# Kernel tuning notes

Hardware: AMD Instinct MI355X
Metric: run time of the kernel (lower is better)

## Reference

```python
import jax, jax.numpy as jnp
import numpy as np

B, NPG = 32, 4096   # graphs, nodes per graph (equal-size ragged segments)
F_IN, C, K, J = 64, 128, 32, 40
N_LAYERS = 3
EPS = 1e-5


def _global_layer_norm(x):
    # F.layer_norm(x, x.shape): normalize over ALL elements, no affine
    m = jnp.mean(x)
    v = jnp.mean(jnp.square(x - m))
    return (x - m) * jax.lax.rsqrt(v + EPS)


def setup_inputs() -> dict:
    key = jax.random.key(0)
    ks = jax.random.split(key, 7)
    N = B * NPG
    return {
        "node_feats": jax.random.normal(ks[0], (N, F_IN), jnp.float32),
        "frag_emb": jax.random.normal(ks[1], (B, J, F_IN), jnp.float32),
        "W_in": jax.random.normal(ks[2], (C, F_IN), jnp.float32) / np.sqrt(F_IN),
        "b_in": jnp.zeros((C,), jnp.float32),
        "U": jax.random.uniform(ks[3], (C, K), jnp.float32),
        "V": jax.random.uniform(ks[4], (C, K), jnp.float32),
        "q": jax.random.uniform(ks[5], (K,), jnp.float32),
        "gate_W": jax.random.normal(ks[6], (1, 2 * C), jnp.float32) / np.sqrt(2 * C),
        "gate_b": jnp.zeros((1,), jnp.float32),
    }


def reference(node_feats, frag_emb, W_in, b_in, U, V, q, gate_W, gate_b):
    # dropout is identity in eval mode
    xs = _global_layer_norm(node_feats @ W_in.T + b_in)      # [N, C]
    ys = _global_layer_norm(frag_emb @ W_in.T + b_in)        # [B, J, C]

    x = xs.reshape(B, NPG, C)                                # ragged segments -> [B, n, C]
    y_p = jax.nn.relu(jnp.einsum('bjd,dk->bjk', ys, V))      # [B, J, K]
    y_p = jax.nn.relu(q * y_p)

    I = x_p = None
    for il in range(N_LAYERS):
        x_p = jax.nn.relu(jnp.einsum('bid,dk->bik', x, U))   # [B, n, K]
        I = jnp.einsum('bik,bjk->bij', x_p, y_p)             # [B, n, J]
        if il < N_LAYERS - 1:
            A = jax.nn.softmax(I, axis=1)                    # softmax over nodes i
            h = jax.nn.relu(jnp.einsum('bij,bjk->bik', A, y_p))
            h = jnp.einsum('bik,dk->bid', h, V)              # [B, n, C]
            z = jax.nn.sigmoid(jnp.concatenate([x, h], -1) @ gate_W.T + gate_b)[..., 0]
            x = (1.0 - z)[..., None] * x + z[..., None] * h

    p = jnp.einsum('bij,bjk->bik', I, y_p)                   # [B, n, K]
    return jax.nn.sigmoid(jnp.einsum('bik,bik->bi', x_p, p)) # [B, n]
```

## Files before the change

kernel.cpp:

```cpp
#include <hip/hip_runtime.h>
#include <math.h>

namespace {
constexpr int BB = 32, NPG = 4096, NTOT = BB*NPG, C = 128, FIN = 64, KK = 32, JJ = 40;
constexpr int YROWS = BB*JJ;
constexpr float EPS = 1e-5f;

constexpr int CW_WU  = 0;
constexpr int CW_WV  = 2048;
constexpr int CW_VU  = 4096;
constexpr int CW_WG  = 5120;
constexpr int CW_VGX = 5184;
constexpr int CW_VGH = 5216;
constexpr int CW_CBU = 5248;
constexpr int CW_CSU = 5280;
constexpr int CW_CBV = 5312;
constexpr int CW_CSV = 5344;
constexpr int CW_SC  = 5376;
constexpr int CW_G   = 5384;
constexpr int CW_WB  = 9480;
constexpr int CW_SW  = 9544;
constexpr int CW_SB  = 9608;
constexpr int CW_SIZE = 9610;

constexpr size_t XU_OFF  = 0;
constexpr size_t GX_OFF  = XU_OFF + (size_t)NTOT*KK;
constexpr size_t YP_OFF  = GX_OFF + (size_t)NTOT;
constexpr size_t PMA_OFF = YP_OFF + (size_t)YROWS*KK;
constexpr size_t PSA_OFF = PMA_OFF + 81920;
constexpr size_t PMB_OFF = PSA_OFF + 81920;
constexpr size_t PSB_OFF = PMB_OFF + 81920;
constexpr size_t CWS_OFF = PSB_OFF + 81920;
constexpr size_t PBN_OFF = CWS_OFF + 9612;
constexpr size_t PBF_OFF = PBN_OFF + 2048;
constexpr size_t MS_OFF  = PBF_OFF + 80;
constexpr size_t ST_OFF  = MS_OFF + 2560;
constexpr size_t IBF_OFF = ST_OFF + 8;
}

#define ACC8(A, wv, u0, u1) do { \
  A[0] += (wv)*(u0).x; A[1] += (wv)*(u0).y; A[2] += (wv)*(u0).z; A[3] += (wv)*(u0).w; \
  A[4] += (wv)*(u1).x; A[5] += (wv)*(u1).y; A[6] += (wv)*(u1).z; A[7] += (wv)*(u1).w; } while(0)

__device__ __forceinline__ float dot4(const float4 a, const float4 b) {
  return a.x*b.x + a.y*b.y + a.z*b.z + a.w*b.w;
}
__device__ __forceinline__ float dot8v(const float x[8], const float4 y0, const float4 y1) {
  return x[0]*y0.x + x[1]*y0.y + x[2]*y0.z + x[3]*y0.w
       + x[4]*y1.x + x[5]*y1.y + x[6]*y1.z + x[7]*y1.w;
}
__device__ __forceinline__ float sigm(const float x) { return 1.f/(1.f + __expf(-x)); }

__global__ __launch_bounds__(256)
void k_pre(const float* __restrict__ W, const float* __restrict__ b,
           const float* __restrict__ U, const float* __restrict__ V,
           const float* __restrict__ gw, float* __restrict__ CWo) {
  __shared__ float W_l[128*64];
  __shared__ float V_l[128*32];
  const int t = threadIdx.x;
  for (int f = t; f < 2048; f += 256) *(float4*)(W_l + 4*f) = *(const float4*)(W + 4*f);
  if (blockIdx.x == 0)
    for (int f = t; f < 1024; f += 256) *(float4*)(V_l + 4*f) = *(const float4*)(V + 4*f);
  __syncthreads();
  if (blockIdx.x == 1) {
    const int d = t >> 2, e0 = (t & 3) * 16;
    float g[16];
    #pragma unroll
    for (int i = 0; i < 16; ++i) g[i] = 0.f;
    for (int c = 0; c < 128; ++c) {
      const float wv = W_l[c*64 + d];
      #pragma unroll
      for (int u = 0; u < 4; ++u) {
        const float4 we = *(const float4*)(W_l + c*64 + e0 + 4*u);
        g[4*u+0] += wv*we.x; g[4*u+1] += wv*we.y;
        g[4*u+2] += wv*we.z; g[4*u+3] += wv*we.w;
      }
    }
    #pragma unroll
    for (int u = 0; u < 4; ++u)
      *(float4*)(CWo + CW_G + d*64 + e0 + 4*u) = make_float4(g[4*u],g[4*u+1],g[4*u+2],g[4*u+3]);
    if (t < 64) {
      float awb = 0.f, asw = 0.f;
      for (int c = 0; c < 128; ++c) {
        const float wv = W_l[c*64 + t];
        awb += wv * b[c]; asw += wv;
      }
      CWo[CW_WB + t] = awb; CWo[CW_SW + t] = asw;
    }
    if (t == 0) {
      float sb = 0.f, sb2 = 0.f;
      for (int c = 0; c < 128; ++c) { sb += b[c]; sb2 += b[c]*b[c]; }
      CWo[CW_SB+0] = sb; CWo[CW_SB+1] = sb2;
    }
    return;
  }
  {
    const int d = t >> 2, k0 = (t & 3) * 8;
    float au[8] = {0,0,0,0,0,0,0,0};
    float av[8] = {0,0,0,0,0,0,0,0};
    for (int c = 0; c < 128; ++c) {
      const float wv = W_l[c*64 + d];
      const float4 u0 = *(const float4*)(U + c*32 + k0);
      const float4 u1 = *(const float4*)(U + c*32 + k0 + 4);
      ACC8(au, wv, u0, u1);
      const float4 v0 = *(const float4*)(V_l + c*32 + k0);
      const float4 v1 = *(const float4*)(V_l + c*32 + k0 + 4);
      ACC8(av, wv, v0, v1);
    }
    *(float4*)(CWo + CW_WU + d*32 + k0)     = make_float4(au[0],au[1],au[2],au[3]);
    *(float4*)(CWo + CW_WU + d*32 + k0 + 4) = make_float4(au[4],au[5],au[6],au[7]);
    *(float4*)(CWo + CW_WV + d*32 + k0)     = make_float4(av[0],av[1],av[2],av[3]);
    *(float4*)(CWo + CW_WV + d*32 + k0 + 4) = make_float4(av[4],av[5],av[6],av[7]);
  }
  if (t < 128) {
    const int kp = t >> 2, k0 = (t & 3) * 8;
    float a[8] = {0,0,0,0,0,0,0,0};
    for (int c = 0; c < 128; ++c) {
      const float vv = V_l[c*32 + kp];
      const float4 u0 = *(const float4*)(U + c*32 + k0);
      const float4 u1 = *(const float4*)(U + c*32 + k0 + 4);
      ACC8(a, vv, u0, u1);
    }
    *(float4*)(CWo + CW_VU + kp*32 + k0)     = make_float4(a[0],a[1],a[2],a[3]);
    *(float4*)(CWo + CW_VU + kp*32 + k0 + 4) = make_float4(a[4],a[5],a[6],a[7]);
  }
  if (t < 64) {
    float a = 0.f;
    for (int c = 0; c < 128; ++c) a += W_l[c*64 + t] * gw[c];
    CWo[CW_WG + t] = a;
  }
  if (t < 32) {
    float a1=0,a2=0,a3=0,a4=0,a5=0,a6=0;
    for (int c = 0; c < 128; ++c) {
      const float uv = U[c*32 + t], vv = V_l[c*32 + t], bc = b[c];
      a1 += vv*gw[c]; a2 += vv*gw[128+c];
      a3 += bc*uv;    a4 += uv;
      a5 += bc*vv;    a6 += vv;
    }
    CWo[CW_VGX+t]=a1; CWo[CW_VGH+t]=a2; CWo[CW_CBU+t]=a3; CWo[CW_CSU+t]=a4;
    CWo[CW_CBV+t]=a5; CWo[CW_CSV+t]=a6;
  }
  if (t == 0) {
    float bg=0.f, sg=0.f;
    for (int c = 0; c < 128; ++c) { bg += b[c]*gw[c]; sg += gw[c]; }
    CWo[CW_SC+0]=bg; CWo[CW_SC+1]=sg;
  }
}

__global__ __launch_bounds__(256,6)
void k_cov(const float* __restrict__ inp, const float* __restrict__ CW,
           double* __restrict__ PB, const int ntiles) {
  __shared__ float a_l[64*64];
  __shared__ float red[12];
  const int t = threadIdx.x;
  const int dg = t >> 4, eg = t & 15;
  const int d0 = dg*4, e0 = eg*4;
  float av1 = 0.f, av2 = 0.f, avb = 0.f;
  int nt = 0;
  for (int tile = blockIdx.x; tile < ntiles; tile += gridDim.x) {
    __syncthreads();
    const size_t r0 = (size_t)tile * 64;
    #pragma unroll
    for (int s = 0; s < 4; ++s) {
      int f = (t + 256*s) * 4;
      *(float4*)(a_l + f) = *(const float4*)(inp + r0*FIN + f);
    }
    __syncthreads();
    float S[4][4];
    #pragma unroll
    for (int i=0;i<4;i++)
      #pragma unroll
      for (int j=0;j<4;j++) S[i][j] = 0.f;
    float4 cs = make_float4(0.f,0.f,0.f,0.f);
    #pragma unroll 4
    for (int r = 0; r < 64; ++r) {
      const float4 ad = *(const float4*)(a_l + r*64 + d0);
      const float4 ae = *(const float4*)(a_l + r*64 + e0);
      S[0][0]+=ad.x*ae.x; S[0][1]+=ad.x*ae.y; S[0][2]+=ad.x*ae.z; S[0][3]+=ad.x*ae.w;
      S[1][0]+=ad.y*ae.x; S[1][1]+=ad.y*ae.y; S[1][2]+=ad.y*ae.z; S[1][3]+=ad.y*ae.w;
      S[2][0]+=ad.z*ae.x; S[2][1]+=ad.z*ae.y; S[2][2]+=ad.z*ae.z; S[2][3]+=ad.z*ae.w;
      S[3][0]+=ad.w*ae.x; S[3][1]+=ad.w*ae.y; S[3][2]+=ad.w*ae.z; S[3][3]+=ad.w*ae.w;
      cs.x += ad.x; cs.y += ad.y; cs.z += ad.z; cs.w += ad.w;
    }
    #pragma unroll
    for (int i = 0; i < 4; ++i) {
      const float4 g4 = *(const float4*)(CW + CW_G + (d0+i)*64 + e0);
      av2 += S[i][0]*g4.x + S[i][1]*g4.y + S[i][2]*g4.z + S[i][3]*g4.w;
    }
    if (eg == 0) {
      const float4 sw4 = *(const float4*)(CW + CW_SW + d0);
      const float4 wb4 = *(const float4*)(CW + CW_WB + d0);
      av1 += cs.x*sw4.x + cs.y*sw4.y + cs.z*sw4.z + cs.w*sw4.w;
      avb += cs.x*wb4.x + cs.y*wb4.y + cs.z*wb4.z + cs.w*wb4.w;
    }
    ++nt;
  }
  #pragma unroll
  for (int off = 32; off > 0; off >>= 1) {
    av2 += __shfl_xor(av2, off);
    av1 += __shfl_xor(av1, off);
    avb += __shfl_xor(avb, off);
  }
  const int w = t >> 6;
  if ((t & 63) == 0) { red[w*3] = av1; red[w*3+1] = av2; red[w*3+2] = avb; }
  __syncthreads();
  if (t == 0) {
    const float sb = CW[CW_SB], sb2 = CW[CW_SB+1];
    const double rowsB = 64.0 * (double)nt;
    const double s1 = (double)(red[0]+red[3]+red[6]+red[9]);
    const double s2 = (double)(red[1]+red[4]+red[7]+red[10]);
    const double sB = (double)(red[2]+red[5]+red[8]+red[11]);
    PB[(size_t)blockIdx.x*2 + 0] = s1 + rowsB*(double)sb;
    PB[(size_t)blockIdx.x*2 + 1] = s2 + 2.0*sB + rowsB*(double)sb2;
  }
}

__global__ __launch_bounds__(256)
void k_comb(const double* __restrict__ PBn, const double* __restrict__ PBf,
            double* __restrict__ ST) {
  __shared__ double red[8];
  const int t = threadIdx.x;
  double a = PBn[2*t] + PBn[2*(t+256)];
  double b = PBn[2*t+1] + PBn[2*(t+256)+1];
  #pragma unroll
  for (int off = 32; off > 0; off >>= 1) {
    a += __shfl_down(a, off);
    b += __shfl_down(b, off);
  }
  if ((t & 63) == 0) { red[(t>>6)*2] = a; red[(t>>6)*2+1] = b; }
  __syncthreads();
  if (t == 0) {
    ST[0] = red[0]+red[2]+red[4]+red[6];
    ST[1] = red[1]+red[3]+red[5]+red[7];
  }
  if (t < 64) {
    double c = (t < 20) ? PBf[2*t]   : 0.0;
    double d = (t < 20) ? PBf[2*t+1] : 0.0;
    #pragma unroll
    for (int off = 32; off > 0; off >>= 1) {
      c += __shfl_down(c, off);
      d += __shfl_down(d, off);
    }
    if (t == 0) { ST[2] = c; ST[3] = d; }
  }
}

__global__ __launch_bounds__(256)
void k_comb2(const float* __restrict__ Pm, const float* __restrict__ Ps,
             float* __restrict__ MS) {
  __shared__ float Mq[160], Sq[160], Msh[40];
  const int t = threadIdx.x;
  const int b = blockIdx.x;
  const int j = t >> 2, q = t & 3;
  float pm[16];
  if (t < 160) {
    float m = 0.f;
    #pragma unroll
    for (int u = 0; u < 16; ++u) {
      pm[u] = Pm[(size_t)b*2560 + j*64 + q*16 + u];
      m = fmaxf(m, pm[u]);
    }
    Mq[t] = m;
  }
  __syncthreads();
  if (t < 40) Msh[t] = fmaxf(fmaxf(Mq[4*t], Mq[4*t+1]), fmaxf(Mq[4*t+2], Mq[4*t+3]));
  __syncthreads();
  if (t < 160) {
    const float M = Msh[j];
    float s = 0.f;
    #pragma unroll
    for (int u = 0; u < 16; ++u)
      s += Ps[(size_t)b*2560 + j*64 + q*16 + u] * __expf(pm[u] - M);
    Sq[t] = s;
  }
  __syncthreads();
  if (t < 40) {
    const float S = Sq[4*t] + Sq[4*t+1] + Sq[4*t+2] + Sq[4*t+3];
    MS[(size_t)b*80 + t] = Msh[t];
    MS[(size_t)b*80 + 40 + t] = 1.f/S;
  }
}

__device__ __forceinline__ void irow_compute(const float* ypj, const float xp[8],
                                             const int kq, float4 p[10]) {
  #pragma unroll
  for (int m = 0; m < 10; ++m) {
    float4 acc;
    #pragma unroll
    for (int jj = 0; jj < 4; ++jj) {
      const int j = 4*m + jj;
      const float4 y0 = *(const float4*)(ypj + j*32 + kq*8);
      const float4 y1 = *(const float4*)(ypj + j*32 + kq*8 + 4);
      const float s = xp[0]*y0.x + xp[1]*y0.y + xp[2]*y0.z + xp[3]*y0.w
                    + xp[4]*y1.x + xp[5]*y1.y + xp[6]*y1.z + xp[7]*y1.w;
      if (jj==0) acc.x = s; else if (jj==1) acc.y = s; else if (jj==2) acc.z = s; else acc.w = s;
    }
    acc.x += __shfl_xor(acc.x,1); acc.x += __shfl_xor(acc.x,2);
    acc.y += __shfl_xor(acc.y,1); acc.y += __shfl_xor(acc.y,2);
    acc.z += __shfl_xor(acc.z,1); acc.z += __shfl_xor(acc.z,2);
    acc.w += __shfl_xor(acc.w,1); acc.w += __shfl_xor(acc.w,2);
    p[m] = acc;
  }
}

__device__ __forceinline__ void partials_out(const float4 p[10], const int t, const int kq,
    float* sredm, float* sreds, float* redm,
    float* __restrict__ PmB, float* __restrict__ PsB) {
  float ev[10];
  #pragma unroll
  for (int m = 0; m < 10; ++m) {
    const float4 qv = p[m];
    ev[m] = (kq&1) ? ((kq&2)? qv.w : qv.y) : ((kq&2)? qv.z : qv.x);
  }
  const int w = t >> 6, tl = t & 63;
  float mv[10];
  #pragma unroll
  for (int m = 0; m < 10; ++m) {
    mv[m] = ev[m];
    mv[m] = fmaxf(mv[m], __shfl_xor(mv[m], 4));
    mv[m] = fmaxf(mv[m], __shfl_xor(mv[m], 8));
    mv[m] = fmaxf(mv[m], __shfl_xor(mv[m], 16));
    mv[m] = fmaxf(mv[m], __shfl_xor(mv[m], 32));
  }
  if (tl < 4) {
    #pragma unroll
    for (int m = 0; m < 10; ++m) sredm[w*40 + 4*m + kq] = mv[m];
  }
  __syncthreads();
  if (t < 40)
    redm[t] = fmaxf(fmaxf(sredm[t], sredm[40+t]), fmaxf(sredm[80+t], sredm[120+t]));
  __syncthreads();
  float es[10];
  #pragma unroll
  for (int m = 0; m < 10; ++m) {
    const float M = redm[4*m + kq];
    es[m] = __expf(ev[m]-M);
    es[m] += __shfl_xor(es[m], 4);
    es[m] += __shfl_xor(es[m], 8);
    es[m] += __shfl_xor(es[m], 16);
    es[m] += __shfl_xor(es[m], 32);
  }
  if (tl < 4) {
    #pragma unroll
    for (int m = 0; m < 10; ++m) sreds[w*40 + 4*m + kq] = es[m];
  }
  __syncthreads();
  if (t < 40) {
    PmB[(size_t)t*64] = redm[t];
    PsB[(size_t)t*64] = sreds[t]+sreds[40+t]+sreds[80+t]+sreds[120+t];
  }
}

__device__ __forceinline__ void partials_lds(const float* p_l, const int t,
    float* sredm, float* sreds, float* redm,
    float* __restrict__ PmB, float* __restrict__ PsB) {
  const int r2 = t >> 2, kq = t & 3;
  const int w = t >> 6, tl = t & 63;
  float ev[10];
  #pragma unroll
  for (int m = 0; m < 10; ++m) ev[m] = p_l[r2*44 + 4*m + kq];
  float mv[10];
  #pragma unroll
  for (int m = 0; m < 10; ++m) {
    mv[m] = ev[m];
    mv[m] = fmaxf(mv[m], __shfl_xor(mv[m], 4));
    mv[m] = fmaxf(mv[m], __shfl_xor(mv[m], 8));
    mv[m] = fmaxf(mv[m], __shfl_xor(mv[m], 16));
    mv[m] = fmaxf(mv[m], __shfl_xor(mv[m], 32));
  }
  if (tl < 4) {
    #pragma unroll
    for (int m = 0; m < 10; ++m) sredm[w*40 + 4*m + kq] = mv[m];
  }
  __syncthreads();
  if (t < 40)
    redm[t] = fmaxf(fmaxf(sredm[t], sredm[40+t]), fmaxf(sredm[80+t], sredm[120+t]));
  __syncthreads();
  float es[10];
  #pragma unroll
  for (int m = 0; m < 10; ++m) {
    const float M = redm[4*m + kq];
    es[m] = __expf(ev[m]-M);
    es[m] += __shfl_xor(es[m], 4);
    es[m] += __shfl_xor(es[m], 8);
    es[m] += __shfl_xor(es[m], 16);
    es[m] += __shfl_xor(es[m], 32);
  }
  if (tl < 4) {
    #pragma unroll
    for (int m = 0; m < 10; ++m) sreds[w*40 + 4*m + kq] = es[m];
  }
  __syncthreads();
  if (t < 40) {
    PmB[(size_t)t*64] = redm[t];
    PsB[(size_t)t*64] = sreds[t]+sreds[40+t]+sreds[80+t]+sreds[120+t];
  }
}

__global__ __launch_bounds__(256,4)
void k_yp2(const float* __restrict__ fe, const float* __restrict__ CW,
           const float* __restrict__ q, const double* __restrict__ ST,
           float* __restrict__ yp) {
  __shared__ float in_t[64*64];
  __shared__ float Wl[64*32];
  const int t = threadIdx.x;
  const int r0 = blockIdx.x * 64;
  #pragma unroll
  for (int s = 0; s < 4; ++s) {
    int f = (t + 256*s) * 4;
    int r = f >> 6, d = f & 63;
    float4 v = *(const float4*)(fe + (size_t)r0*FIN + f);
    *(float4*)(in_t + r*64 + (d ^ ((r & 7) * 8))) = v;
  }
  #pragma unroll
  for (int s = 0; s < 2; ++s) {
    int f = (t + 256*s) * 4;
    *(float4*)(Wl + f) = *(const float4*)(CW + CW_WV + f);
  }
  __syncthreads();
  const double cy = (double)YROWS * (double)C;
  const double myd = ST[2]/cy, vy = ST[3]/cy - myd*myd;
  const float ry = (float)(1.0/sqrt(vy + (double)EPS));
  const float mr = (float)myd * ry;
  const int r2 = t >> 2, kq = t & 3;
  const int swz = (r2 & 7) * 8;
  float acc[8] = {0,0,0,0,0,0,0,0};
  #pragma unroll
  for (int dc = 0; dc < 16; ++dc) {
    const int d = dc*4;
    const float4 a = *(const float4*)(in_t + r2*64 + (d ^ swz));
    { const float4 w0 = *(const float4*)(Wl + (d+0)*32 + kq*8);
      const float4 w1 = *(const float4*)(Wl + (d+0)*32 + kq*8 + 4); ACC8(acc, a.x, w0, w1); }
    { const float4 w0 = *(const float4*)(Wl + (d+1)*32 + kq*8);
      const float4 w1 = *(const float4*)(Wl + (d+1)*32 + kq*8 + 4); ACC8(acc, a.y, w0, w1); }
    { const float4 w0 = *(const float4*)(Wl + (d+2)*32 + kq*8);
      const float4 w1 = *(const float4*)(Wl + (d+2)*32 + kq*8 + 4); ACC8(acc, a.z, w0, w1); }
    { const float4 w0 = *(const float4*)(Wl + (d+3)*32 + kq*8);
      const float4 w1 = *(const float4*)(Wl + (d+3)*32 + kq*8 + 4); ACC8(acc, a.w, w0, w1); }
  }
  #pragma unroll
  for (int i = 0; i < 8; ++i) {
    const int k = kq*8 + i;
    const float typ = ry*(acc[i] + CW[CW_CBV+k]) - mr*CW[CW_CSV+k];
    float v = fmaxf(typ, 0.f);
    acc[i] = fmaxf(q[k]*v, 0.f);
  }
  *(float4*)(yp + (size_t)(r0+r2)*KK + kq*8)     = make_float4(acc[0],acc[1],acc[2],acc[3]);
  *(float4*)(yp + (size_t)(r0+r2)*KK + kq*8 + 4) = make_float4(acc[4],acc[5],acc[6],acc[7]);
}

__global__ __launch_bounds__(256,4)
void k_I0b(const float* __restrict__ nf, const float* __restrict__ CW,
           const double* __restrict__ ST, const float* __restrict__ yp,
           float* __restrict__ XU, float* __restrict__ GX,
           float* __restrict__ Pm, float* __restrict__ Ps,
           float* __restrict__ Ibf) {
  __shared__ __align__(16) float in_t[64*68];
  __shared__ __align__(16) float Wl[64*36];
  __shared__ __align__(16) float ypj[40*40];
  __shared__ __align__(16) float wgl[64];
  __shared__ float sredm[160], sreds[160], redm[40];
  float* p_l = in_t;
  const int t = threadIdx.x;
  const int bid = blockIdx.x;
  const int b = bid >> 6, blk = bid & 63;
  const size_t rowbase = (size_t)b*NPG + (size_t)blk*64;
  #pragma unroll
  for (int s = 0; s < 4; ++s) {
    int f = (t + 256*s) * 4;
    int r = f >> 6, d = f & 63;
    *(float4*)(in_t + r*68 + d) = *(const float4*)(nf + rowbase*FIN + f);
  }
  #pragma unroll
  for (int s = 0; s < 2; ++s) {
    int idx = t + 256*s;
    int d = idx >> 3, kc = idx & 7;
    *(float4*)(Wl + ((d&15)*4 + (d>>4))*36 + kc*4) = *(const float4*)(CW + CW_WU + idx*4);
  }
  for (int f4v = t; f4v < 320; f4v += 256) {
    int j = f4v >> 3, kc = f4v & 7;
    *(float4*)(ypj + j*40 + kc*4) = *(const float4*)(yp + (size_t)b*(JJ*KK) + f4v*4);
  }
  if (t < 64) wgl[t] = CW[CW_WG + t];
  __syncthreads();
  const double cx = (double)NTOT * (double)C;
  const double mx = ST[0]/cx, vx = ST[1]/cx - mx*mx;
  const float rx = (float)(1.0/sqrt(vx + (double)EPS));
  const float mr = (float)mx * rx;
  const int kq = t & 3, X = (t >> 2) & 3, rr = t >> 4;
  float acc[4][8];
  #pragma unroll
  for (int i=0;i<4;i++)
    #pragma unroll
    for (int u=0;u<8;u++) acc[i][u] = 0.f;
  #pragma unroll
  for (int dd = 0; dd < 4; ++dd) {
    float4 a4[4];
    #pragma unroll
    for (int i = 0; i < 4; ++i)
      a4[i] = *(const float4*)(in_t + (rr+16*i)*68 + X*16 + dd*4);
    #pragma unroll
    for (int qd = 0; qd < 4; ++qd) {
      const int lrow = (dd*4 + qd)*4 + X;
      const float4 w0 = *(const float4*)(Wl + lrow*36 + kq*8);
      const float4 w1 = *(const float4*)(Wl + lrow*36 + kq*8 + 4);
      #pragma unroll
      for (int i = 0; i < 4; ++i) {
        const float av = (qd==0)? a4[i].x : (qd==1)? a4[i].y : (qd==2)? a4[i].z : a4[i].w;
        ACC8(acc[i], av, w0, w1);
      }
    }
  }
  #pragma unroll
  for (int i = 0; i < 4; ++i)
    #pragma unroll
    for (int u = 0; u < 8; ++u) {
      acc[i][u] += __shfl_xor(acc[i][u], 4);
      acc[i][u] += __shfl_xor(acc[i][u], 8);
    }
  float gp[4];
  #pragma unroll
  for (int i = 0; i < 4; ++i) {
    const float4 a = *(const float4*)(in_t + (rr+16*i)*68 + X*16 + kq*4);
    const float4 w = *(const float4*)(wgl + X*16 + kq*4);
    gp[i] = dot4(a, w);
    gp[i] += __shfl_xor(gp[i], 1);
    gp[i] += __shfl_xor(gp[i], 2);
    gp[i] += __shfl_xor(gp[i], 4);
    gp[i] += __shfl_xor(gp[i], 8);
  }
  const float4 cb0 = *(const float4*)(CW + CW_CBU + kq*8);
  const float4 cb1 = *(const float4*)(CW + CW_CBU + kq*8 + 4);
  const float4 cu0 = *(const float4*)(CW + CW_CSU + kq*8);
  const float4 cu1 = *(const float4*)(CW + CW_CSU + kq*8 + 4);
  float xp[4][8];
  #pragma unroll
  for (int i = 0; i < 4; ++i) {
    acc[i][0] = rx*(acc[i][0] + cb0.x) - mr*cu0.x;
    acc[i][1] = rx*(acc[i][1] + cb0.y) - mr*cu0.y;
    acc[i][2] = rx*(acc[i][2] + cb0.z) - mr*cu0.z;
    acc[i][3] = rx*(acc[i][3] + cb0.w) - mr*cu0.w;
    acc[i][4] = rx*(acc[i][4] + cb1.x) - mr*cu1.x;
    acc[i][5] = rx*(acc[i][5] + cb1.y) - mr*cu1.y;
    acc[i][6] = rx*(acc[i][6] + cb1.z) - mr*cu1.z;
    acc[i][7] = rx*(acc[i][7] + cb1.w) - mr*cu1.w;
    #pragma unroll
    for (int u = 0; u < 8; ++u) xp[i][u] = fmaxf(acc[i][u], 0.f);
  }
  if (X == 0) {
    const float bG = CW[CW_SC], sG = CW[CW_SC+1];
    #pragma unroll
    for (int i = 0; i < 4; ++i) {
      const size_t row = rowbase + rr + 16*i;
      *(float4*)(XU + row*KK + kq*8)     = make_float4(acc[i][0],acc[i][1],acc[i][2],acc[i][3]);
      *(float4*)(XU + row*KK + kq*8 + 4) = make_float4(acc[i][4],acc[i][5],acc[i][6],acc[i][7]);
      if (kq == 0) GX[row] = rx*(gp[i] + bG) - mr*sG;
    }
  }
  __syncthreads();
  #pragma unroll 2
  for (int jj = 0; jj < 10; ++jj) {
    const int j = X*10 + jj;
    const float4 y0 = *(const float4*)(ypj + j*40 + kq*8);
    const float4 y1 = *(const float4*)(ypj + j*40 + kq*8 + 4);
    float p4[4];
    #pragma unroll
    for (int i = 0; i < 4; ++i) p4[i] = dot8v(xp[i], y0, y1);
    #pragma unroll
    for (int i = 0; i < 4; ++i) {
      p4[i] += __shfl_xor(p4[i], 1);
      p4[i] += __shfl_xor(p4[i], 2);
    }
    if (kq == 0) {
      #pragma unroll
      for (int i = 0; i < 4; ++i)
        p_l[(rr+16*i)*44 + j] = p4[i];
    }
  }
  __syncthreads();
  partials_lds(p_l, t, sredm, sreds, redm,
               Pm + (size_t)b*2560 + blk, Ps + (size_t)b*2560 + blk);
  for (int f4v = t; f4v < 640; f4v += 256) {
    const int row = f4v / 10, jq = f4v - row*10;
    *(float4*)(Ibf + (rowbase+row)*JJ + jq*4) = *(const float4*)(p_l + row*44 + jq*4);
  }
}

template<int FINAL>
__global__ __launch_bounds__(256,4)
void k_fused6(float* __restrict__ XU, float* __restrict__ GX,
              float* __restrict__ Ibf,
              const float* __restrict__ yp, const float* __restrict__ CW,
              const float* __restrict__ gb, const float* __restrict__ MS,
              float* __restrict__ PmOut, float* __restrict__ PsOut,
              float* __restrict__ outp) {
  __shared__ float ypj[40*32];
  __shared__ float e_l[64*44];
  __shared__ float h_l[64*40];
  __shared__ float VUl[32*32];
  __shared__ float M_l[40], Si_l[40];
  __shared__ float vgxl[32], vghl[32];
  float* sredm = e_l;
  float* sreds = e_l + 160;
  float* redm  = e_l + 320;
  const int t = threadIdx.x;
  const int bid = blockIdx.x;
  const int b = bid >> 6, blk = bid & 63;
  const size_t rowbase = (size_t)b*NPG + (size_t)blk*64;
  for (int f4v = t; f4v < 320; f4v += 256)
    *(float4*)(ypj + f4v*4) = *(const float4*)(yp + (size_t)b*(JJ*KK) + f4v*4);
  { const int f = t*4;
    *(float4*)(VUl + f) = *(const float4*)(CW + CW_VU + f); }
  if (t < 32) { vgxl[t] = CW[CW_VGX+t]; vghl[t] = CW[CW_VGH+t]; }
  if (t < 40) { M_l[t] = MS[(size_t)b*80 + t]; Si_l[t] = MS[(size_t)b*80 + 40 + t]; }
  __syncthreads();
  for (int f4v = t; f4v < 640; f4v += 256) {
    const int row = f4v / 10, jq = f4v - row*10;
    const float4 iv = *(const float4*)(Ibf + (rowbase+row)*JJ + jq*4);
    float4 e4;
    e4.x = __expf(iv.x - M_l[jq*4+0]) * Si_l[jq*4+0];
    e4.y = __expf(iv.y - M_l[jq*4+1]) * Si_l[jq*4+1];
    e4.z = __expf(iv.z - M_l[jq*4+2]) * Si_l[jq*4+2];
    e4.w = __expf(iv.w - M_l[jq*4+3]) * Si_l[jq*4+3];
    *(float4*)(e_l + row*44 + jq*4) = e4;
  }
  const int r2 = t >> 2, kq = t & 3;
  float xu[8];
  {
    const float4 x0 = *(const float4*)(XU + (rowbase+r2)*KK + kq*8);
    const float4 x1 = *(const float4*)(XU + (rowbase+r2)*KK + kq*8 + 4);
    xu[0]=x0.x; xu[1]=x0.y; xu[2]=x0.z; xu[3]=x0.w;
    xu[4]=x1.x; xu[5]=x1.y; xu[6]=x1.z; xu[7]=x1.w;
  }
  const float gx = GX[rowbase + r2];
  __syncthreads();
  {
    const int rq = t >> 3, kc = t & 7;
    float4 h0 = make_float4(0.f,0.f,0.f,0.f), h1 = make_float4(0.f,0.f,0.f,0.f);
    #pragma unroll 4
    for (int j = 0; j < JJ; ++j) {
      const float4 yv = *(const float4*)(ypj + j*32 + kc*4);
      const float e0 = e_l[rq*44 + j];
      const float e1 = e_l[(rq+32)*44 + j];
      h0.x += e0*yv.x; h0.y += e0*yv.y; h0.z += e0*yv.z; h0.w += e0*yv.w;
      h1.x += e1*yv.x; h1.y += e1*yv.y; h1.z += e1*yv.z; h1.w += e1*yv.w;
    }
    h0.x = fmaxf(h0.x,0.f); h0.y = fmaxf(h0.y,0.f); h0.z = fmaxf(h0.z,0.f); h0.w = fmaxf(h0.w,0.f);
    h1.x = fmaxf(h1.x,0.f); h1.y = fmaxf(h1.y,0.f); h1.z = fmaxf(h1.z,0.f); h1.w = fmaxf(h1.w,0.f);
    *(float4*)(h_l + rq*40 + kc*4) = h0;
    *(float4*)(h_l + (rq+32)*40 + kc*4) = h1;
  }
  __syncthreads();
  float hu[8] = {0,0,0,0,0,0,0,0};
  float gh2 = 0.f, ghx = 0.f;
  #pragma unroll 8
  for (int kp = 0; kp < KK; ++kp) {
    const float hv = h_l[r2*40 + kp];
    gh2 += hv * vghl[kp];
    ghx += hv * vgxl[kp];
    const float4 v0 = *(const float4*)(VUl + kp*32 + kq*8);
    const float4 v1 = *(const float4*)(VUl + kp*32 + kq*8 + 4);
    ACC8(hu, hv, v0, v1);
  }
  const float z = 1.f/(1.f + __expf(-(gx + gh2 + gb[0])));
  float xp[8];
  #pragma unroll
  for (int i = 0; i < 8; ++i) {
    xu[i] = (1.f - z)*xu[i] + z*hu[i];
    xp[i] = fmaxf(xu[i], 0.f);
  }
  if (!FINAL) {
    *(float4*)(XU + (rowbase+r2)*KK + kq*8)     = make_float4(xu[0],xu[1],xu[2],xu[3]);
    *(float4*)(XU + (rowbase+r2)*KK + kq*8 + 4) = make_float4(xu[4],xu[5],xu[6],xu[7]);
    if (kq == 0) GX[rowbase + r2] = (1.f - z)*gx + z*ghx;
  }
  float4 p[10];
  irow_compute(ypj, xp, kq, p);
  if (FINAL) {
    float s = 0.f;
    #pragma unroll
    for (int m = 0; m < 10; ++m)
      s += p[m].x*p[m].x + p[m].y*p[m].y + p[m].z*p[m].z + p[m].w*p[m].w;
    if (kq == 0) outp[rowbase + r2] = 1.f/(1.f + __expf(-s));
    return;
  }
  #pragma unroll
  for (int m = 0; m < 10; ++m)
    if ((m & 3) == kq)
      *(float4*)(Ibf + (rowbase+r2)*JJ + 4*m) = p[m];
  partials_out(p, t, kq, sredm, sreds, redm,
               PmOut + (size_t)b*2560 + blk, PsOut + (size_t)b*2560 + blk);
}

extern "C" void kernel_launch(void* const* d_in, const int* in_sizes, int n_in,
                              void* d_out, int out_size, void* d_ws, size_t ws_size,
                              hipStream_t stream) {
  const float* nf  = (const float*)d_in[0];
  const float* fe  = (const float*)d_in[1];
  const float* W   = (const float*)d_in[2];
  const float* bin = (const float*)d_in[3];
  const float* U   = (const float*)d_in[4];
  const float* V   = (const float*)d_in[5];
  const float* q   = (const float*)d_in[6];
  const float* gw  = (const float*)d_in[7];
  const float* gb  = (const float*)d_in[8];
  float* out = (float*)d_out;
  float* wf  = (float*)d_ws;

  float* XU  = wf + XU_OFF;
  float* GX  = wf + GX_OFF;
  float* YP  = wf + YP_OFF;
  float* PMa = wf + PMA_OFF;
  float* PSa = wf + PSA_OFF;
  float* PMb = wf + PMB_OFF;
  float* PSb = wf + PSB_OFF;
  float* CWp = wf + CWS_OFF;
  float* MSb = wf + MS_OFF;
  float* IBF = wf + IBF_OFF;
  double* PBn = (double*)(wf + PBN_OFF);
  double* PBf = (double*)(wf + PBF_OFF);
  double* ST  = (double*)(wf + ST_OFF);

  k_pre<<<2, 256, 0, stream>>>(W, bin, U, V, gw, CWp);
  k_cov<<<512, 256, 0, stream>>>(nf, CWp, PBn, NTOT/64);
  k_cov<<<20, 256, 0, stream>>>(fe, CWp, PBf, YROWS/64);
  k_comb<<<1, 256, 0, stream>>>(PBn, PBf, ST);
  k_yp2<<<YROWS/64, 256, 0, stream>>>(fe, CWp, q, ST, YP);
  k_I0b<<<NTOT/64, 256, 0, stream>>>(nf, CWp, ST, YP, XU, GX, PMa, PSa, IBF);
  k_comb2<<<32, 256, 0, stream>>>(PMa, PSa, MSb);
  k_fused6<0><<<NTOT/64, 256, 0, stream>>>(XU, GX, IBF, YP, CWp, gb, MSb, PMb, PSb, nullptr);
  k_comb2<<<32, 256, 0, stream>>>(PMb, PSb, MSb);
  k_fused6<1><<<NTOT/64, 256, 0, stream>>>(XU, GX, IBF, YP, CWp, gb, MSb, nullptr, nullptr, out);
}
```

Measured before the change: 254.7 us.

## Fuse small reduction kernels into consumers and merge covariance launches

Merges the two covariance-statistics launches into one grid and folds the global-stats combine kernel into the consumers (yp and I0), where each block redoes the small reduction itself. The per-graph softmax max/sum combine kernel is likewise removed: each fused block recomputes M and 1/S from the partials, which are now stored in a block-major layout. The e matrix in LDS is transposed with padding to avoid bank conflicts. This cuts four launches and their serialization gaps, at the cost of redundant small reductions in every block of the large kernels.

```diff
diff --git a/kernel.cpp b/kernel.cpp
--- a/kernel.cpp
+++ b/kernel.cpp
@@ -33,9 +33,7 @@
 constexpr size_t CWS_OFF = PSB_OFF + 81920;
 constexpr size_t PBN_OFF = CWS_OFF + 9612;
 constexpr size_t PBF_OFF = PBN_OFF + 2048;
-constexpr size_t MS_OFF  = PBF_OFF + 80;
-constexpr size_t ST_OFF  = MS_OFF + 2560;
-constexpr size_t IBF_OFF = ST_OFF + 8;
+constexpr size_t IBF_OFF = PBF_OFF + 80;
 }
 
 #define ACC8(A, wv, u0, u1) do { \
@@ -148,16 +146,23 @@
 }
 
 __global__ __launch_bounds__(256,6)
-void k_cov(const float* __restrict__ inp, const float* __restrict__ CW,
-           double* __restrict__ PB, const int ntiles) {
+void k_cov2(const float* __restrict__ nf, const float* __restrict__ fe,
+            const float* __restrict__ CW,
+            double* __restrict__ PBn, double* __restrict__ PBf) {
   __shared__ float a_l[64*64];
   __shared__ float red[12];
   const int t = threadIdx.x;
+  const bool isNf = (blockIdx.x < 512);
+  const float* inp = isNf ? nf : fe;
+  double* PB = isNf ? PBn : PBf;
+  const int bid = isNf ? blockIdx.x : (blockIdx.x - 512);
+  const int ntiles = isNf ? (NTOT/64) : (YROWS/64);
+  const int gstr = isNf ? 512 : 20;
   const int dg = t >> 4, eg = t & 15;
   const int d0 = dg*4, e0 = eg*4;
   float av1 = 0.f, av2 = 0.f, avb = 0.f;
   int nt = 0;
-  for (int tile = blockIdx.x; tile < ntiles; tile += gridDim.x) {
+  for (int tile = bid; tile < ntiles; tile += gstr) {
     __syncthreads();
     const size_t r0 = (size_t)tile * 64;
     #pragma unroll
@@ -210,74 +215,8 @@
     const double s1 = (double)(red[0]+red[3]+red[6]+red[9]);
     const double s2 = (double)(red[1]+red[4]+red[7]+red[10]);
     const double sB = (double)(red[2]+red[5]+red[8]+red[11]);
-    PB[(size_t)blockIdx.x*2 + 0] = s1 + rowsB*(double)sb;
-    PB[(size_t)blockIdx.x*2 + 1] = s2 + 2.0*sB + rowsB*(double)sb2;
-  }
-}
-
-__global__ __launch_bounds__(256)
-void k_comb(const double* __restrict__ PBn, const double* __restrict__ PBf,
-            double* __restrict__ ST) {
-  __shared__ double red[8];
-  const int t = threadIdx.x;
-  double a = PBn[2*t] + PBn[2*(t+256)];
-  double b = PBn[2*t+1] + PBn[2*(t+256)+1];
-  #pragma unroll
-  for (int off = 32; off > 0; off >>= 1) {
-    a += __shfl_down(a, off);
-    b += __shfl_down(b, off);
-  }
-  if ((t & 63) == 0) { red[(t>>6)*2] = a; red[(t>>6)*2+1] = b; }
-  __syncthreads();
-  if (t == 0) {
-    ST[0] = red[0]+red[2]+red[4]+red[6];
-    ST[1] = red[1]+red[3]+red[5]+red[7];
-  }
-  if (t < 64) {
-    double c = (t < 20) ? PBf[2*t]   : 0.0;
-    double d = (t < 20) ? PBf[2*t+1] : 0.0;
-    #pragma unroll
-    for (int off = 32; off > 0; off >>= 1) {
-      c += __shfl_down(c, off);
-      d += __shfl_down(d, off);
-    }
-    if (t == 0) { ST[2] = c; ST[3] = d; }
-  }
-}
-
-__global__ __launch_bounds__(256)
-void k_comb2(const float* __restrict__ Pm, const float* __restrict__ Ps,
-             float* __restrict__ MS) {
-  __shared__ float Mq[160], Sq[160], Msh[40];
-  const int t = threadIdx.x;
-  const int b = blockIdx.x;
-  const int j = t >> 2, q = t & 3;
-  float pm[16];
-  if (t < 160) {
-    float m = 0.f;
-    #pragma unroll
-    for (int u = 0; u < 16; ++u) {
-      pm[u] = Pm[(size_t)b*2560 + j*64 + q*16 + u];
-      m = fmaxf(m, pm[u]);
-    }
-    Mq[t] = m;
-  }
-  __syncthreads();
-  if (t < 40) Msh[t] = fmaxf(fmaxf(Mq[4*t], Mq[4*t+1]), fmaxf(Mq[4*t+2], Mq[4*t+3]));
-  __syncthreads();
-  if (t < 160) {
-    const float M = Msh[j];
-    float s = 0.f;
-    #pragma unroll
-    for (int u = 0; u < 16; ++u)
-      s += Ps[(size_t)b*2560 + j*64 + q*16 + u] * __expf(pm[u] - M);
-    Sq[t] = s;
-  }
-  __syncthreads();
-  if (t < 40) {
-    const float S = Sq[4*t] + Sq[4*t+1] + Sq[4*t+2] + Sq[4*t+3];
-    MS[(size_t)b*80 + t] = Msh[t];
-    MS[(size_t)b*80 + 40 + t] = 1.f/S;
+    PB[(size_t)bid*2 + 0] = s1 + rowsB*(double)sb;
+    PB[(size_t)bid*2 + 1] = s2 + 2.0*sB + rowsB*(double)sb2;
   }
 }
 
@@ -346,8 +285,8 @@
   }
   __syncthreads();
   if (t < 40) {
-    PmB[(size_t)t*64] = redm[t];
-    PsB[(size_t)t*64] = sreds[t]+sreds[40+t]+sreds[80+t]+sreds[120+t];
+    PmB[t] = redm[t];
+    PsB[t] = sreds[t]+sreds[40+t]+sreds[80+t]+sreds[120+t];
   }
 }
 
@@ -392,17 +331,18 @@
   }
   __syncthreads();
   if (t < 40) {
-    PmB[(size_t)t*64] = redm[t];
-    PsB[(size_t)t*64] = sreds[t]+sreds[40+t]+sreds[80+t]+sreds[120+t];
+    PmB[t] = redm[t];
+    PsB[t] = sreds[t]+sreds[40+t]+sreds[80+t]+sreds[120+t];
   }
 }
 
 __global__ __launch_bounds__(256,4)
-void k_yp2(const float* __restrict__ fe, const float* __restrict__ CW,
-           const float* __restrict__ q, const double* __restrict__ ST,
+void k_yp3(const float* __restrict__ fe, const float* __restrict__ CW,
+           const float* __restrict__ q, const double* __restrict__ PBf,
            float* __restrict__ yp) {
   __shared__ float in_t[64*64];
   __shared__ float Wl[64*32];
+  __shared__ double fred[2];
   const int t = threadIdx.x;
   const int r0 = blockIdx.x * 64;
   #pragma unroll
@@ -417,9 +357,19 @@
     int f = (t + 256*s) * 4;
     *(float4*)(Wl + f) = *(const float4*)(CW + CW_WV + f);
   }
+  if (t < 64) {
+    double c = (t < 20) ? PBf[2*t]   : 0.0;
+    double d = (t < 20) ? PBf[2*t+1] : 0.0;
+    #pragma unroll
+    for (int off = 32; off > 0; off >>= 1) {
+      c += __shfl_down(c, off);
+      d += __shfl_down(d, off);
+    }
+    if (t == 0) { fred[0] = c; fred[1] = d; }
+  }
   __syncthreads();
   const double cy = (double)YROWS * (double)C;
-  const double myd = ST[2]/cy, vy = ST[3]/cy - myd*myd;
+  const double myd = fred[0]/cy, vy = fred[1]/cy - myd*myd;
   const float ry = (float)(1.0/sqrt(vy + (double)EPS));
   const float mr = (float)myd * ry;
   const int r2 = t >> 2, kq = t & 3;
@@ -450,8 +400,8 @@
 }
 
 __global__ __launch_bounds__(256,4)
-void k_I0b(const float* __restrict__ nf, const float* __restrict__ CW,
-           const double* __restrict__ ST, const float* __restrict__ yp,
+void k_I0c(const float* __restrict__ nf, const float* __restrict__ CW,
+           const double* __restrict__ PBn, const float* __restrict__ yp,
            float* __restrict__ XU, float* __restrict__ GX,
            float* __restrict__ Pm, float* __restrict__ Ps,
            float* __restrict__ Ibf) {
@@ -460,6 +410,7 @@
   __shared__ __align__(16) float ypj[40*40];
   __shared__ __align__(16) float wgl[64];
   __shared__ float sredm[160], sreds[160], redm[40];
+  __shared__ double dred[8];
   float* p_l = in_t;
   const int t = threadIdx.x;
   const int bid = blockIdx.x;
@@ -482,9 +433,21 @@
     *(float4*)(ypj + j*40 + kc*4) = *(const float4*)(yp + (size_t)b*(JJ*KK) + f4v*4);
   }
   if (t < 64) wgl[t] = CW[CW_WG + t];
-  __syncthreads();
+  {
+    double a = PBn[2*t] + PBn[2*(t+256)];
+    double bb = PBn[2*t+1] + PBn[2*(t+256)+1];
+    #pragma unroll
+    for (int off = 32; off > 0; off >>= 1) {
+      a  += __shfl_down(a, off);
+      bb += __shfl_down(bb, off);
+    }
+    if ((t & 63) == 0) { dred[(t>>6)*2] = a; dred[(t>>6)*2+1] = bb; }
+  }
+  __syncthreads();
+  const double ST0 = dred[0]+dred[2]+dred[4]+dred[6];
+  const double ST1 = dred[1]+dred[3]+dred[5]+dred[7];
   const double cx = (double)NTOT * (double)C;
-  const double mx = ST[0]/cx, vx = ST[1]/cx - mx*mx;
+  const double mx = ST0/cx, vx = ST1/cx - mx*mx;
   const float rx = (float)(1.0/sqrt(vx + (double)EPS));
   const float mr = (float)mx * rx;
   const int kq = t & 3, X = (t >> 2) & 3, rr = t >> 4;
@@ -579,7 +542,7 @@
   }
   __syncthreads();
   partials_lds(p_l, t, sredm, sreds, redm,
-               Pm + (size_t)b*2560 + blk, Ps + (size_t)b*2560 + blk);
+               Pm + ((size_t)b*64 + blk)*40, Ps + ((size_t)b*64 + blk)*40);
   for (int f4v = t; f4v < 640; f4v += 256) {
     const int row = f4v / 10, jq = f4v - row*10;
     *(float4*)(Ibf + (rowbase+row)*JJ + jq*4) = *(const float4*)(p_l + row*44 + jq*4);
@@ -588,21 +551,23 @@
 
 template<int FINAL>
 __global__ __launch_bounds__(256,4)
-void k_fused6(float* __restrict__ XU, float* __restrict__ GX,
+void k_fused7(float* __restrict__ XU, float* __restrict__ GX,
               float* __restrict__ Ibf,
               const float* __restrict__ yp, const float* __restrict__ CW,
-              const float* __restrict__ gb, const float* __restrict__ MS,
+              const float* __restrict__ gb,
+              const float* __restrict__ PmIn, const float* __restrict__ PsIn,
               float* __restrict__ PmOut, float* __restrict__ PsOut,
               float* __restrict__ outp) {
   __shared__ float ypj[40*32];
-  __shared__ float e_l[64*44];
+  __shared__ float eT[40*65];
   __shared__ float h_l[64*40];
   __shared__ float VUl[32*32];
   __shared__ float M_l[40], Si_l[40];
   __shared__ float vgxl[32], vghl[32];
-  float* sredm = e_l;
-  float* sreds = e_l + 160;
-  float* redm  = e_l + 320;
+  __shared__ float Mq[160], Sq[160];
+  float* sredm = eT;
+  float* sreds = eT + 160;
+  float* redm  = eT + 320;
   const int t = threadIdx.x;
   const int bid = blockIdx.x;
   const int b = bid >> 6, blk = bid & 63;
@@ -612,17 +577,38 @@
   { const int f = t*4;
     *(float4*)(VUl + f) = *(const float4*)(CW + CW_VU + f); }
   if (t < 32) { vgxl[t] = CW[CW_VGX+t]; vghl[t] = CW[CW_VGH+t]; }
-  if (t < 40) { M_l[t] = MS[(size_t)b*80 + t]; Si_l[t] = MS[(size_t)b*80 + 40 + t]; }
+  const int j160 = t >> 2, q160 = t & 3;
+  float pmv[16];
+  if (t < 160) {
+    float m = 0.f;
+    #pragma unroll
+    for (int u = 0; u < 16; ++u) {
+      pmv[u] = PmIn[((size_t)b*64 + q160*16 + u)*40 + j160];
+      m = fmaxf(m, pmv[u]);
+    }
+    Mq[t] = m;
+  }
+  __syncthreads();
+  if (t < 40) M_l[t] = fmaxf(fmaxf(Mq[4*t], Mq[4*t+1]), fmaxf(Mq[4*t+2], Mq[4*t+3]));
+  __syncthreads();
+  if (t < 160) {
+    const float M = M_l[j160];
+    float s = 0.f;
+    #pragma unroll
+    for (int u = 0; u < 16; ++u)
+      s += PsIn[((size_t)b*64 + q160*16 + u)*40 + j160] * __expf(pmv[u] - M);
+    Sq[t] = s;
+  }
+  __syncthreads();
+  if (t < 40) Si_l[t] = 1.f/(Sq[4*t] + Sq[4*t+1] + Sq[4*t+2] + Sq[4*t+3]);
   __syncthreads();
   for (int f4v = t; f4v < 640; f4v += 256) {
     const int row = f4v / 10, jq = f4v - row*10;
     const float4 iv = *(const float4*)(Ibf + (rowbase+row)*JJ + jq*4);
-    float4 e4;
-    e4.x = __expf(iv.x - M_l[jq*4+0]) * Si_l[jq*4+0];
-    e4.y = __expf(iv.y - M_l[jq*4+1]) * Si_l[jq*4+1];
-    e4.z = __expf(iv.z - M_l[jq*4+2]) * Si_l[jq*4+2];
-    e4.w = __expf(iv.w - M_l[jq*4+3]) * Si_l[jq*4+3];
-    *(float4*)(e_l + row*44 + jq*4) = e4;
+    eT[(jq*4+0)*65 + row] = __expf(iv.x - M_l[jq*4+0]) * Si_l[jq*4+0];
+    eT[(jq*4+1)*65 + row] = __expf(iv.y - M_l[jq*4+1]) * Si_l[jq*4+1];
+    eT[(jq*4+2)*65 + row] = __expf(iv.z - M_l[jq*4+2]) * Si_l[jq*4+2];
+    eT[(jq*4+3)*65 + row] = __expf(iv.w - M_l[jq*4+3]) * Si_l[jq*4+3];
   }
   const int r2 = t >> 2, kq = t & 3;
   float xu[8];
@@ -640,8 +626,8 @@
     #pragma unroll 4
     for (int j = 0; j < JJ; ++j) {
       const float4 yv = *(const float4*)(ypj + j*32 + kc*4);
-      const float e0 = e_l[rq*44 + j];
-      const float e1 = e_l[(rq+32)*44 + j];
+      const float e0 = eT[j*65 + rq];
+      const float e1 = eT[j*65 + rq + 32];
       h0.x += e0*yv.x; h0.y += e0*yv.y; h0.z += e0*yv.z; h0.w += e0*yv.w;
       h1.x += e1*yv.x; h1.y += e1*yv.y; h1.z += e1*yv.z; h1.w += e1*yv.w;
     }
@@ -689,7 +675,7 @@
     if ((m & 3) == kq)
       *(float4*)(Ibf + (rowbase+r2)*JJ + 4*m) = p[m];
   partials_out(p, t, kq, sredm, sreds, redm,
-               PmOut + (size_t)b*2560 + blk, PsOut + (size_t)b*2560 + blk);
+               PmOut + ((size_t)b*64 + blk)*40, PsOut + ((size_t)b*64 + blk)*40);
 }
 
 extern "C" void kernel_launch(void* const* d_in, const int* in_sizes, int n_in,
@@ -715,20 +701,14 @@
   float* PMb = wf + PMB_OFF;
   float* PSb = wf + PSB_OFF;
   float* CWp = wf + CWS_OFF;
-  float* MSb = wf + MS_OFF;
   float* IBF = wf + IBF_OFF;
   double* PBn = (double*)(wf + PBN_OFF);
   double* PBf = (double*)(wf + PBF_OFF);
-  double* ST  = (double*)(wf + ST_OFF);
 
   k_pre<<<2, 256, 0, stream>>>(W, bin, U, V, gw, CWp);
-  k_cov<<<512, 256, 0, stream>>>(nf, CWp, PBn, NTOT/64);
-  k_cov<<<20, 256, 0, stream>>>(fe, CWp, PBf, YROWS/64);
-  k_comb<<<1, 256, 0, stream>>>(PBn, PBf, ST);
-  k_yp2<<<YROWS/64, 256, 0, stream>>>(fe, CWp, q, ST, YP);
-  k_I0b<<<NTOT/64, 256, 0, stream>>>(nf, CWp, ST, YP, XU, GX, PMa, PSa, IBF);
-  k_comb2<<<32, 256, 0, stream>>>(PMa, PSa, MSb);
-  k_fused6<0><<<NTOT/64, 256, 0, stream>>>(XU, GX, IBF, YP, CWp, gb, MSb, PMb, PSb, nullptr);
-  k_comb2<<<32, 256, 0, stream>>>(PMb, PSb, MSb);
-  k_fused6<1><<<NTOT/64, 256, 0, stream>>>(XU, GX, IBF, YP, CWp, gb, MSb, nullptr, nullptr, out);
-}
+  k_cov2<<<532, 256, 0, stream>>>(nf, fe, CWp, PBn, PBf);
+  k_yp3<<<YROWS/64, 256, 0, stream>>>(fe, CWp, q, PBf, YP);
+  k_I0c<<<NTOT/64, 256, 0, stream>>>(nf, CWp, PBn, YP, XU, GX, PMa, PSa, IBF);
+  k_fused7<0><<<NTOT/64, 256, 0, stream>>>(XU, GX, IBF, YP, CWp, gb, PMa, PSa, PMb, PSb, nullptr);
+  k_fused7<1><<<NTOT/64, 256, 0, stream>>>(XU, GX, IBF, YP, CWp, gb, PMb, PSb, nullptr, nullptr, out);
+}
```

After: 249.1 us. 2.2% less time.
